# Optimization experiments

Hardware: AMD Instinct MI355X
Metric: run time of the kernel (lower is better)

The kernel has to match this reference:

```python
import jax, jax.numpy as jnp
import numpy as np

_N = 512
_L = 65536


def setup_inputs() -> dict:
    key = jax.random.key(0)
    ks = jax.random.split(key, 11)
    N, L = _N, _L
    sc = 1.0 / np.sqrt(N)  # lecun-normal style scaling
    f = lambda k, s: jax.random.normal(k, s, dtype=jnp.float32)
    return {
        # stable DPLR spectrum: negative real parts
        "Lambda_re": -(jax.random.uniform(ks[0], (N,), dtype=jnp.float32) + 0.1),
        "Lambda_im": f(ks[1], (N,)),
        "p_re": f(ks[2], (N,)), "p_im": f(ks[3], (N,)),
        "q_re": f(ks[4], (N,)), "q_im": f(ks[5], (N,)),
        "Vc_re": f(ks[6], (N, N)) * sc, "Vc_im": f(ks[7], (N, N)) * sc,
        "Ct": f(ks[8], (1, N, 2)) * sc,
        "B": f(ks[9], (N, 1)) * sc,
        "log_step": jax.random.uniform(ks[10], (1,), dtype=jnp.float32)
                    * (np.log(0.1) - np.log(0.001)) + np.log(0.001),
        "L": L,
    }


def reference(Lambda_re, Lambda_im, p_re, p_im, q_re, q_im,
              Vc_re, Vc_im, Ct, B, log_step, L):
    Lambda = Lambda_re + 1j * Lambda_im            # (N,)
    p = p_re + 1j * p_im                           # (N,)
    q = q_re + 1j * q_im                           # (N,)
    Vc = Vc_re + 1j * Vc_im                        # (N,N)
    Ct_c = Ct[..., 0] + 1j * Ct[..., 1]            # (1,N)
    Bc = (Vc @ B.astype(Vc.dtype)).ravel()         # (N,) complex, B = Vc @ B
    step = jnp.exp(log_step)[0]

    # aterm = (Ct*, q*), bterm = (B, p)
    a0 = Ct_c.conj().ravel()
    a1 = q.conj()
    b0 = Bc
    b1 = p

    # roots of unity
    Omega = jnp.exp(-2j * jnp.pi * (jnp.arange(L) / L))   # (L,)
    g = (2.0 / step) * ((1.0 - Omega) / (1.0 + Omega))    # (L,) bilinear transform
    c = 2.0 / (1.0 + Omega)                               # (L,)

    # single fused Cauchy pass: resolvent (L,N) contracted with all 4 rank-1 terms
    r = 1.0 / (g[:, None] - Lambda[None, :])               # (L,N)
    terms = jnp.stack([a0 * b0, a0 * b1, a1 * b0, a1 * b1], axis=1)  # (N,4)
    K = r @ terms                                          # (L,4): k00,k01,k10,k11
    k00, k01, k10, k11 = K[:, 0], K[:, 1], K[:, 2], K[:, 3]

    atRoots = c * (k00 - k01 * (1.0 / (1.0 + k11)) * k10)  # Woodbury correction
    out = jnp.fft.ifft(atRoots, L).reshape(L)
    return out.real
```

## Files before the change

kernel.cpp:

```cpp
#include <hip/hip_runtime.h>
#include <math.h>

constexpr int WS_TERMS = 0;
constexpr int WS_ZT    = 8192;

__global__ __launch_bounds__(256) void k_setup(
    const float* __restrict__ Lr, const float* __restrict__ Li,
    const float* __restrict__ pr, const float* __restrict__ pi,
    const float* __restrict__ qr, const float* __restrict__ qi,
    const float* __restrict__ Vr, const float* __restrict__ Vi,
    const float* __restrict__ Ct, const float* __restrict__ Bv,
    float* __restrict__ terms)
{
    __shared__ float red[8];
    int n = blockIdx.x;
    int t = threadIdx.x;
    float b0 = Bv[t], b1 = Bv[t + 256];
    float sr = fmaf(Vr[n*512 + t], b0, Vr[n*512 + t + 256] * b1);
    float si = fmaf(Vi[n*512 + t], b0, Vi[n*512 + t + 256] * b1);
    #pragma unroll
    for (int off = 32; off > 0; off >>= 1) {
        sr += __shfl_down(sr, off, 64);
        si += __shfl_down(si, off, 64);
    }
    if ((t & 63) == 0) { red[(t >> 6)*2] = sr; red[(t >> 6)*2 + 1] = si; }
    __syncthreads();
    if (t == 0) {
        float b0r = red[0] + red[2] + red[4] + red[6];
        float b0i = red[1] + red[3] + red[5] + red[7];
        float a0r = Ct[2*n], a0i = -Ct[2*n+1];
        float a1r = qr[n],   a1i = -qi[n];
        float b1r = pr[n],   b1i = pi[n];
        float* tm = terms + n * 12;
        tm[0]  = Lr[n];                tm[1]  = Li[n];
        tm[2]  = a0r*b0r - a0i*b0i;    tm[3]  = a0r*b0i + a0i*b0r;
        tm[4]  = a0r*b1r - a0i*b1i;    tm[5]  = a0r*b1i + a0i*b1r;
        tm[6]  = a1r*b0r - a1i*b0i;    tm[7]  = a1r*b0i + a1i*b0r;
        tm[8]  = a1r*b1r - a1i*b1i;    tm[9]  = a1r*b1i + a1i*b1r;
        tm[10] = 0.f;                  tm[11] = 0.f;
    }
}

__global__ __launch_bounds__(1024, 8) void k_mainA(
    const float* __restrict__ terms,
    const float* __restrict__ log_step,
    float* __restrict__ ZTf)
{
    __shared__ float buf[11520];
    int tid = threadIdx.x;
    int l1  = blockIdx.x;

    {
        float4* dst = (float4*)buf;
        const float4* src = (const float4*)terms;
        for (int i = tid; i < 1536; i += 1024) dst[i] = src[i];
    }

    int u     = tid & 127;
    int chunk = tid >> 7;

    double step = exp((double)log_step[0]);
    double t2s  = 2.0 / step;
    double th0  = -6.283185307179586 * ((double)(l1 + 256*u) / 65536.0);
    float gr[2], gi[2], cr_[2], ci_[2];
    #pragma unroll
    for (int h = 0; h < 2; ++h) {
        double th = th0 - 3.141592653589793 * (double)h;
        double sn, cn; sincos(th, &sn, &cn);
        double A = 1.0 - cn, C = 1.0 + cn, Bm = -sn, D = sn;
        double inv = 1.0 / (C*C + D*D);
        gr[h]  = (float)(t2s * (A*C + Bm*D) * inv);
        gi[h]  = (float)(t2s * (Bm*C - A*D) * inv);
        cr_[h] = (float)(2.0 * C * inv);
        ci_[h] = (float)(-2.0 * D * inv);
    }
    __syncthreads();

    float ac[2][8];
    #pragma unroll
    for (int h = 0; h < 2; ++h)
        #pragma unroll
        for (int c = 0; c < 8; ++c) ac[h][c] = 0.f;

    const float4* t4 = (const float4*)buf + chunk * 64 * 3;
    #pragma unroll 2
    for (int n = 0; n < 64; ++n) {
        float4 Aq = t4[n*3 + 0];
        float4 Bq = t4[n*3 + 1];
        float4 Cq = t4[n*3 + 2];
        #pragma unroll
        for (int h = 0; h < 2; ++h) {
            float dr = gr[h] - Aq.x;
            float di = gi[h] - Aq.y;
            float dd = fmaf(dr, dr, di * di);
            float iv = __builtin_amdgcn_rcpf(dd);
            float rr = dr * iv;
            float ri = -di * iv;
            ac[h][0] = fmaf(rr, Aq.z, ac[h][0]); ac[h][0] = fmaf(-ri, Aq.w, ac[h][0]);
            ac[h][1] = fmaf(rr, Aq.w, ac[h][1]); ac[h][1] = fmaf( ri, Aq.z, ac[h][1]);
            ac[h][2] = fmaf(rr, Bq.x, ac[h][2]); ac[h][2] = fmaf(-ri, Bq.y, ac[h][2]);
            ac[h][3] = fmaf(rr, Bq.y, ac[h][3]); ac[h][3] = fmaf( ri, Bq.x, ac[h][3]);
            ac[h][4] = fmaf(rr, Bq.z, ac[h][4]); ac[h][4] = fmaf(-ri, Bq.w, ac[h][4]);
            ac[h][5] = fmaf(rr, Bq.w, ac[h][5]); ac[h][5] = fmaf( ri, Bq.z, ac[h][5]);
            ac[h][6] = fmaf(rr, Cq.x, ac[h][6]); ac[h][6] = fmaf(-ri, Cq.y, ac[h][6]);
            ac[h][7] = fmaf(rr, Cq.y, ac[h][7]); ac[h][7] = fmaf( ri, Cq.x, ac[h][7]);
        }
    }
    __syncthreads();

    if (chunk >= 4) {
        #pragma unroll
        for (int h = 0; h < 2; ++h) {
            float* p = buf + (chunk - 4) * 2304 + (u + 128*h) * 9;
            #pragma unroll
            for (int c = 0; c < 8; ++c) p[c] = ac[h][c];
        }
    }
    __syncthreads();
    if (chunk < 4) {
        #pragma unroll
        for (int h = 0; h < 2; ++h) {
            float* p = buf + chunk * 2304 + (u + 128*h) * 9;
            #pragma unroll
            for (int c = 0; c < 8; ++c) p[c] += ac[h][c];
        }
    }
    __syncthreads();

    for (int s = tid; s < 2048; s += 1024) {
        int a = (s >> 3) * 9 + (s & 7);
        float v = buf[a] + buf[2304 + a] + buf[4608 + a] + buf[6912 + a];
        buf[9216 + a] = v;
    }
    __syncthreads();

    if (tid < 256) {
        const float* rd = buf + 9216 + tid * 9;
        float s0r = rd[0], s0i = rd[1], s1r = rd[2], s1i = rd[3];
        float s2r = rd[4], s2i = rd[5], s3r = rd[6], s3i = rd[7];
        int h = tid >> 7;
        float e1r = 1.f + s3r, e1i = s3i;
        float eiv = 1.0f / fmaf(e1r, e1r, e1i * e1i);
        float m_r = s1r * s2r - s1i * s2i;
        float m_i = s1r * s2i + s1i * s2r;
        float q_r = (m_r * e1r + m_i * e1i) * eiv;
        float q_i = (m_i * e1r - m_r * e1i) * eiv;
        float u_r = s0r - q_r;
        float u_i = s0i - q_i;
        float at_r = cr_[h] * u_r - ci_[h] * u_i;
        float at_i = cr_[h] * u_i + ci_[h] * u_r;
        ((float2*)buf)[tid] = make_float2(at_r, at_i);
    }
    __syncthreads();

    {
        int k = tid & 255;
        int s = tid >> 8;
        int m0 = (s * k) & 3;
        float curR = (m0 == 0) ? 1.f : (m0 == 2 ? -1.f : 0.f);
        float curI = (m0 == 1) ? 1.f : (m0 == 3 ? -1.f : 0.f);
        double rs, rc;
        sincos(6.283185307179586 * ((double)k / 256.0), &rs, &rc);
        float rotR = (float)rc, rotI = (float)rs;
        const float2* xrow = (const float2*)buf;
        float yr = 0.f, yi = 0.f;
        #pragma unroll 8
        for (int j = s * 64; j < s * 64 + 64; ++j) {
            float2 x = xrow[j];
            yr = fmaf(x.x, curR, yr); yr = fmaf(-x.y, curI, yr);
            yi = fmaf(x.x, curI, yi); yi = fmaf( x.y, curR, yi);
            float nR = curR * rotR - curI * rotI;
            float nI = curR * rotI + curI * rotR;
            curR = nR; curI = nI;
        }
        ((float2*)(buf + 512))[tid] = make_float2(yr, yi);
    }
    __syncthreads();
    if (tid < 256) {
        const float2* pA = (const float2*)(buf + 512);
        float2 p0 = pA[tid], p1 = pA[tid+256], p2 = pA[tid+512], p3 = pA[tid+768];
        float Yr = p0.x + p1.x + p2.x + p3.x;
        float Yi = p0.y + p1.y + p2.y + p3.y;
        int mm = (l1 * tid) & 65535;
        float tv = (float)mm * (1.0f / 65536.0f);
        float twR = __builtin_amdgcn_cosf(tv);
        float twI = __builtin_amdgcn_sinf(tv);
        ((float2*)ZTf)[tid * 256 + l1] =
            make_float2(Yr * twR - Yi * twI, Yr * twI + Yi * twR);
    }
}

__global__ __launch_bounds__(1024) void k_fftB(
    const float* __restrict__ ZTf, float* __restrict__ out)
{
    __shared__ float2 zrow[256];
    __shared__ float partB[1024];
    int t1  = blockIdx.x;
    int tid = threadIdx.x;
    if (tid < 256) zrow[tid] = ((const float2*)ZTf)[t1 * 256 + tid];
    int k   = tid & 255;
    int s   = tid >> 8;
    int m0 = (s * k) & 3;
    float curR = (m0 == 0) ? 1.f : (m0 == 2 ? -1.f : 0.f);
    float curI = (m0 == 1) ? 1.f : (m0 == 3 ? -1.f : 0.f);
    double rs, rc;
    sincos(6.283185307179586 * ((double)k / 256.0), &rs, &rc);
    float rotR = (float)rc, rotI = (float)rs;
    __syncthreads();
    float o = 0.f;
    #pragma unroll 8
    for (int j = s * 64; j < s * 64 + 64; ++j) {
        float2 z = zrow[j];
        o = fmaf(z.x, curR, o);
        o = fmaf(-z.y, curI, o);
        float nR = curR * rotR - curI * rotI;
        float nI = curR * rotI + curI * rotR;
        curR = nR; curI = nI;
    }
    partB[tid] = o;
    __syncthreads();
    if (tid < 256) {
        float sum = partB[tid] + partB[tid+256] + partB[tid+512] + partB[tid+768];
        out[t1 + 256 * tid] = sum * (1.0f / 65536.0f);
    }
}

extern "C" void kernel_launch(void* const* d_in, const int* in_sizes, int n_in,
                              void* d_out, int out_size, void* d_ws, size_t ws_size,
                              hipStream_t stream)
{
    const float* Lambda_re = (const float*)d_in[0];
    const float* Lambda_im = (const float*)d_in[1];
    const float* p_re      = (const float*)d_in[2];
    const float* p_im      = (const float*)d_in[3];
    const float* q_re      = (const float*)d_in[4];
    const float* q_im      = (const float*)d_in[5];
    const float* Vc_re     = (const float*)d_in[6];
    const float* Vc_im     = (const float*)d_in[7];
    const float* Ct        = (const float*)d_in[8];
    const float* Bv        = (const float*)d_in[9];
    const float* log_step  = (const float*)d_in[10];

    float* wsf   = (float*)d_ws;
    float* terms = wsf + WS_TERMS;
    float* ZT    = wsf + WS_ZT;
    float* out   = (float*)d_out;

    k_setup<<<512, 256, 0, stream>>>(Lambda_re, Lambda_im, p_re, p_im, q_re, q_im,
                                     Vc_re, Vc_im, Ct, Bv, terms);
    k_mainA<<<256, 1024, 0, stream>>>(terms, log_step, ZT);
    k_fftB<<<256, 1024, 0, stream>>>(ZT, out);
}
```

Measured before the change: 107.3 us.

## Fuse setup, Cauchy and FFT stages into one cooperative kernel with analytic bilinear simplification

Merges the three kernels into a single cooperative launch that uses grid-wide syncs between the setup, Cauchy/first-FFT and second-FFT phases, which removes two kernel launch gaps. It also simplifies the bilinear transform algebraically: g becomes purely imaginary (t2s·tan), so the resolvent denominator uses a precomputed Lambda_re squared, and c·u becomes (1 + iT)·u. Double-precision sincos is replaced with hardware sin/cos intrinsics. This adds grid-sync overhead and some float precision risk near the tan singularity, which is handled with a clamp.

```diff
diff --git a/kernel.cpp b/kernel.cpp
--- a/kernel.cpp
+++ b/kernel.cpp
@@ -1,86 +1,89 @@
 #include <hip/hip_runtime.h>
+#include <hip/hip_cooperative_groups.h>
 #include <math.h>
+
+namespace cg = cooperative_groups;
 
 constexpr int WS_TERMS = 0;
 constexpr int WS_ZT    = 8192;
 
-__global__ __launch_bounds__(256) void k_setup(
+__device__ __forceinline__ float sin2pi(float x) { return __builtin_amdgcn_sinf(x); }
+__device__ __forceinline__ float cos2pi(float x) { return __builtin_amdgcn_cosf(x); }
+
+__global__ __launch_bounds__(1024, 4) void k_all(
     const float* __restrict__ Lr, const float* __restrict__ Li,
     const float* __restrict__ pr, const float* __restrict__ pi,
     const float* __restrict__ qr, const float* __restrict__ qi,
     const float* __restrict__ Vr, const float* __restrict__ Vi,
     const float* __restrict__ Ct, const float* __restrict__ Bv,
-    float* __restrict__ terms)
-{
-    __shared__ float red[8];
-    int n = blockIdx.x;
-    int t = threadIdx.x;
-    float b0 = Bv[t], b1 = Bv[t + 256];
-    float sr = fmaf(Vr[n*512 + t], b0, Vr[n*512 + t + 256] * b1);
-    float si = fmaf(Vi[n*512 + t], b0, Vi[n*512 + t + 256] * b1);
-    #pragma unroll
-    for (int off = 32; off > 0; off >>= 1) {
-        sr += __shfl_down(sr, off, 64);
-        si += __shfl_down(si, off, 64);
-    }
-    if ((t & 63) == 0) { red[(t >> 6)*2] = sr; red[(t >> 6)*2 + 1] = si; }
-    __syncthreads();
-    if (t == 0) {
-        float b0r = red[0] + red[2] + red[4] + red[6];
-        float b0i = red[1] + red[3] + red[5] + red[7];
-        float a0r = Ct[2*n], a0i = -Ct[2*n+1];
-        float a1r = qr[n],   a1i = -qi[n];
-        float b1r = pr[n],   b1i = pi[n];
-        float* tm = terms + n * 12;
-        tm[0]  = Lr[n];                tm[1]  = Li[n];
-        tm[2]  = a0r*b0r - a0i*b0i;    tm[3]  = a0r*b0i + a0i*b0r;
-        tm[4]  = a0r*b1r - a0i*b1i;    tm[5]  = a0r*b1i + a0i*b1r;
-        tm[6]  = a1r*b0r - a1i*b0i;    tm[7]  = a1r*b0i + a1i*b0r;
-        tm[8]  = a1r*b1r - a1i*b1i;    tm[9]  = a1r*b1i + a1i*b1r;
-        tm[10] = 0.f;                  tm[11] = 0.f;
-    }
-}
-
-__global__ __launch_bounds__(1024, 8) void k_mainA(
-    const float* __restrict__ terms,
     const float* __restrict__ log_step,
-    float* __restrict__ ZTf)
+    float* __restrict__ termsG, float* __restrict__ ZTf,
+    float* __restrict__ out)
 {
     __shared__ float buf[11520];
+    __shared__ float red[16][2];
+    cg::grid_group grid = cg::this_grid();
     int tid = threadIdx.x;
-    int l1  = blockIdx.x;
-
+    int b   = blockIdx.x;
+
+    {
+        int half = tid >> 9;
+        int m    = tid & 511;
+        int n    = 2*b + half;
+        float bv = Bv[m];
+        float sr = Vr[n*512 + m] * bv;
+        float si = Vi[n*512 + m] * bv;
+        #pragma unroll
+        for (int off = 32; off > 0; off >>= 1) {
+            sr += __shfl_down(sr, off, 64);
+            si += __shfl_down(si, off, 64);
+        }
+        if ((tid & 63) == 0) { red[tid >> 6][0] = sr; red[tid >> 6][1] = si; }
+        __syncthreads();
+        if ((tid & 511) == 0) {
+            int wb = half * 8;
+            float b0r = 0.f, b0i = 0.f;
+            #pragma unroll
+            for (int w = 0; w < 8; ++w) { b0r += red[wb+w][0]; b0i += red[wb+w][1]; }
+            double step = exp((double)log_step[0]);
+            float t2s = (float)(2.0 / step);
+            float lr  = Lr[n];
+            float a0r = Ct[2*n], a0i = -Ct[2*n+1];
+            float a1r = qr[n],   a1i = -qi[n];
+            float b1r = pr[n],   b1i = pi[n];
+            float* tm = termsG + n * 12;
+            tm[0]  = -lr;                 tm[1]  = Li[n];
+            tm[2]  = a0r*b0r - a0i*b0i;   tm[3]  = a0r*b0i + a0i*b0r;
+            tm[4]  = a0r*b1r - a0i*b1i;   tm[5]  = a0r*b1i + a0i*b1r;
+            tm[6]  = a1r*b0r - a1i*b0i;   tm[7]  = a1r*b0i + a1i*b0r;
+            tm[8]  = a1r*b1r - a1i*b1i;   tm[9]  = a1r*b1i + a1i*b1r;
+            tm[10] = lr*lr;               tm[11] = t2s;
+        }
+    }
+    grid.sync();
+
+    int l1 = b;
     {
         float4* dst = (float4*)buf;
-        const float4* src = (const float4*)terms;
+        const float4* src = (const float4*)termsG;
         for (int i = tid; i < 1536; i += 1024) dst[i] = src[i];
     }
-
     int u     = tid & 127;
     int chunk = tid >> 7;
 
-    double step = exp((double)log_step[0]);
-    double t2s  = 2.0 / step;
-    double th0  = -6.283185307179586 * ((double)(l1 + 256*u) / 65536.0);
-    float gr[2], gi[2], cr_[2], ci_[2];
+    float tv2 = (float)(l1 + 256*u) * (1.0f / 131072.0f);
+    float sn  = sin2pi(tv2), cn = cos2pi(tv2);
+    float T0  = sn / cn;
+    float T1  = -1.0f / T0;
+    __syncthreads();
+    float t2s = buf[11];
+    float gi0 = t2s * T0, Tc0 = T0;
+    float gi1 = t2s * T1, Tc1 = T1;
+    if (!isfinite(gi1)) { gi1 = 3e30f; Tc1 = 0.f; }
+
+    float2 ac[8];
     #pragma unroll
-    for (int h = 0; h < 2; ++h) {
-        double th = th0 - 3.141592653589793 * (double)h;
-        double sn, cn; sincos(th, &sn, &cn);
-        double A = 1.0 - cn, C = 1.0 + cn, Bm = -sn, D = sn;
-        double inv = 1.0 / (C*C + D*D);
-        gr[h]  = (float)(t2s * (A*C + Bm*D) * inv);
-        gi[h]  = (float)(t2s * (Bm*C - A*D) * inv);
-        cr_[h] = (float)(2.0 * C * inv);
-        ci_[h] = (float)(-2.0 * D * inv);
-    }
-    __syncthreads();
-
-    float ac[2][8];
-    #pragma unroll
-    for (int h = 0; h < 2; ++h)
-        #pragma unroll
-        for (int c = 0; c < 8; ++c) ac[h][c] = 0.f;
+    for (int c = 0; c < 8; ++c) ac[c] = make_float2(0.f, 0.f);
 
     const float4* t4 = (const float4*)buf + chunk * 64 * 3;
     #pragma unroll 2
@@ -88,49 +91,53 @@
         float4 Aq = t4[n*3 + 0];
         float4 Bq = t4[n*3 + 1];
         float4 Cq = t4[n*3 + 2];
+        float di0 = gi0 - Aq.y;
+        float dd0 = fmaf(di0, di0, Cq.z);
+        float iv0 = __builtin_amdgcn_rcpf(dd0);
+        float rr0 = Aq.x * iv0;
+        float ri0 = -di0 * iv0;
+        ac[0].x = fmaf(rr0, Aq.z, ac[0].x); ac[0].x = fmaf(-ri0, Aq.w, ac[0].x);
+        ac[1].x = fmaf(rr0, Aq.w, ac[1].x); ac[1].x = fmaf( ri0, Aq.z, ac[1].x);
+        ac[2].x = fmaf(rr0, Bq.x, ac[2].x); ac[2].x = fmaf(-ri0, Bq.y, ac[2].x);
+        ac[3].x = fmaf(rr0, Bq.y, ac[3].x); ac[3].x = fmaf( ri0, Bq.x, ac[3].x);
+        ac[4].x = fmaf(rr0, Bq.z, ac[4].x); ac[4].x = fmaf(-ri0, Bq.w, ac[4].x);
+        ac[5].x = fmaf(rr0, Bq.w, ac[5].x); ac[5].x = fmaf( ri0, Bq.z, ac[5].x);
+        ac[6].x = fmaf(rr0, Cq.x, ac[6].x); ac[6].x = fmaf(-ri0, Cq.y, ac[6].x);
+        ac[7].x = fmaf(rr0, Cq.y, ac[7].x); ac[7].x = fmaf( ri0, Cq.x, ac[7].x);
+        float di1 = gi1 - Aq.y;
+        float dd1 = fmaf(di1, di1, Cq.z);
+        float iv1 = __builtin_amdgcn_rcpf(dd1);
+        float rr1 = Aq.x * iv1;
+        float ri1 = -di1 * iv1;
+        ac[0].y = fmaf(rr1, Aq.z, ac[0].y); ac[0].y = fmaf(-ri1, Aq.w, ac[0].y);
+        ac[1].y = fmaf(rr1, Aq.w, ac[1].y); ac[1].y = fmaf( ri1, Aq.z, ac[1].y);
+        ac[2].y = fmaf(rr1, Bq.x, ac[2].y); ac[2].y = fmaf(-ri1, Bq.y, ac[2].y);
+        ac[3].y = fmaf(rr1, Bq.y, ac[3].y); ac[3].y = fmaf( ri1, Bq.x, ac[3].y);
+        ac[4].y = fmaf(rr1, Bq.z, ac[4].y); ac[4].y = fmaf(-ri1, Bq.w, ac[4].y);
+        ac[5].y = fmaf(rr1, Bq.w, ac[5].y); ac[5].y = fmaf( ri1, Bq.z, ac[5].y);
+        ac[6].y = fmaf(rr1, Cq.x, ac[6].y); ac[6].y = fmaf(-ri1, Cq.y, ac[6].y);
+        ac[7].y = fmaf(rr1, Cq.y, ac[7].y); ac[7].y = fmaf( ri1, Cq.x, ac[7].y);
+    }
+    __syncthreads();
+
+    if (chunk >= 4) {
+        float* p0 = buf + (chunk - 4) * 2304 + u * 9;
+        float* p1 = buf + (chunk - 4) * 2304 + (u + 128) * 9;
         #pragma unroll
-        for (int h = 0; h < 2; ++h) {
-            float dr = gr[h] - Aq.x;
-            float di = gi[h] - Aq.y;
-            float dd = fmaf(dr, dr, di * di);
-            float iv = __builtin_amdgcn_rcpf(dd);
-            float rr = dr * iv;
-            float ri = -di * iv;
-            ac[h][0] = fmaf(rr, Aq.z, ac[h][0]); ac[h][0] = fmaf(-ri, Aq.w, ac[h][0]);
-            ac[h][1] = fmaf(rr, Aq.w, ac[h][1]); ac[h][1] = fmaf( ri, Aq.z, ac[h][1]);
-            ac[h][2] = fmaf(rr, Bq.x, ac[h][2]); ac[h][2] = fmaf(-ri, Bq.y, ac[h][2]);
-            ac[h][3] = fmaf(rr, Bq.y, ac[h][3]); ac[h][3] = fmaf( ri, Bq.x, ac[h][3]);
-            ac[h][4] = fmaf(rr, Bq.z, ac[h][4]); ac[h][4] = fmaf(-ri, Bq.w, ac[h][4]);
-            ac[h][5] = fmaf(rr, Bq.w, ac[h][5]); ac[h][5] = fmaf( ri, Bq.z, ac[h][5]);
-            ac[h][6] = fmaf(rr, Cq.x, ac[h][6]); ac[h][6] = fmaf(-ri, Cq.y, ac[h][6]);
-            ac[h][7] = fmaf(rr, Cq.y, ac[h][7]); ac[h][7] = fmaf( ri, Cq.x, ac[h][7]);
-        }
-    }
-    __syncthreads();
-
-    if (chunk >= 4) {
+        for (int c = 0; c < 8; ++c) { p0[c] = ac[c].x; p1[c] = ac[c].y; }
+    }
+    __syncthreads();
+    if (chunk < 4) {
+        float* p0 = buf + chunk * 2304 + u * 9;
+        float* p1 = buf + chunk * 2304 + (u + 128) * 9;
         #pragma unroll
-        for (int h = 0; h < 2; ++h) {
-            float* p = buf + (chunk - 4) * 2304 + (u + 128*h) * 9;
-            #pragma unroll
-            for (int c = 0; c < 8; ++c) p[c] = ac[h][c];
-        }
-    }
-    __syncthreads();
-    if (chunk < 4) {
-        #pragma unroll
-        for (int h = 0; h < 2; ++h) {
-            float* p = buf + chunk * 2304 + (u + 128*h) * 9;
-            #pragma unroll
-            for (int c = 0; c < 8; ++c) p[c] += ac[h][c];
-        }
+        for (int c = 0; c < 8; ++c) { p0[c] += ac[c].x; p1[c] += ac[c].y; }
     }
     __syncthreads();
 
     for (int s = tid; s < 2048; s += 1024) {
         int a = (s >> 3) * 9 + (s & 7);
-        float v = buf[a] + buf[2304 + a] + buf[4608 + a] + buf[6912 + a];
-        buf[9216 + a] = v;
+        buf[9216 + a] = buf[a] + buf[2304 + a] + buf[4608 + a] + buf[6912 + a];
     }
     __syncthreads();
 
@@ -138,7 +145,7 @@
         const float* rd = buf + 9216 + tid * 9;
         float s0r = rd[0], s0i = rd[1], s1r = rd[2], s1i = rd[3];
         float s2r = rd[4], s2i = rd[5], s3r = rd[6], s3i = rd[7];
-        int h = tid >> 7;
+        float T = (tid >> 7) ? Tc1 : Tc0;
         float e1r = 1.f + s3r, e1i = s3i;
         float eiv = 1.0f / fmaf(e1r, e1r, e1i * e1i);
         float m_r = s1r * s2r - s1i * s2i;
@@ -147,9 +154,7 @@
         float q_i = (m_i * e1r - m_r * e1i) * eiv;
         float u_r = s0r - q_r;
         float u_i = s0i - q_i;
-        float at_r = cr_[h] * u_r - ci_[h] * u_i;
-        float at_i = cr_[h] * u_i + ci_[h] * u_r;
-        ((float2*)buf)[tid] = make_float2(at_r, at_i);
+        ((float2*)buf)[tid] = make_float2(u_r - T * u_i, u_i + T * u_r);
     }
     __syncthreads();
 
@@ -159,9 +164,8 @@
         int m0 = (s * k) & 3;
         float curR = (m0 == 0) ? 1.f : (m0 == 2 ? -1.f : 0.f);
         float curI = (m0 == 1) ? 1.f : (m0 == 3 ? -1.f : 0.f);
-        double rs, rc;
-        sincos(6.283185307179586 * ((double)k / 256.0), &rs, &rc);
-        float rotR = (float)rc, rotI = (float)rs;
+        float rotR = cos2pi((float)k * (1.0f / 256.0f));
+        float rotI = sin2pi((float)k * (1.0f / 256.0f));
         const float2* xrow = (const float2*)buf;
         float yr = 0.f, yi = 0.f;
         #pragma unroll 8
@@ -183,45 +187,40 @@
         float Yi = p0.y + p1.y + p2.y + p3.y;
         int mm = (l1 * tid) & 65535;
         float tv = (float)mm * (1.0f / 65536.0f);
-        float twR = __builtin_amdgcn_cosf(tv);
-        float twI = __builtin_amdgcn_sinf(tv);
+        float twR = cos2pi(tv), twI = sin2pi(tv);
         ((float2*)ZTf)[tid * 256 + l1] =
             make_float2(Yr * twR - Yi * twI, Yr * twI + Yi * twR);
     }
-}
-
-__global__ __launch_bounds__(1024) void k_fftB(
-    const float* __restrict__ ZTf, float* __restrict__ out)
-{
-    __shared__ float2 zrow[256];
-    __shared__ float partB[1024];
-    int t1  = blockIdx.x;
-    int tid = threadIdx.x;
-    if (tid < 256) zrow[tid] = ((const float2*)ZTf)[t1 * 256 + tid];
-    int k   = tid & 255;
-    int s   = tid >> 8;
-    int m0 = (s * k) & 3;
-    float curR = (m0 == 0) ? 1.f : (m0 == 2 ? -1.f : 0.f);
-    float curI = (m0 == 1) ? 1.f : (m0 == 3 ? -1.f : 0.f);
-    double rs, rc;
-    sincos(6.283185307179586 * ((double)k / 256.0), &rs, &rc);
-    float rotR = (float)rc, rotI = (float)rs;
-    __syncthreads();
-    float o = 0.f;
-    #pragma unroll 8
-    for (int j = s * 64; j < s * 64 + 64; ++j) {
-        float2 z = zrow[j];
-        o = fmaf(z.x, curR, o);
-        o = fmaf(-z.y, curI, o);
-        float nR = curR * rotR - curI * rotI;
-        float nI = curR * rotI + curI * rotR;
-        curR = nR; curI = nI;
-    }
-    partB[tid] = o;
-    __syncthreads();
-    if (tid < 256) {
-        float sum = partB[tid] + partB[tid+256] + partB[tid+512] + partB[tid+768];
-        out[t1 + 256 * tid] = sum * (1.0f / 65536.0f);
+    grid.sync();
+
+    {
+        int t1 = b;
+        if (tid < 256) ((float2*)buf)[tid] = ((const float2*)ZTf)[t1 * 256 + tid];
+        int k = tid & 255;
+        int s = tid >> 8;
+        int m0 = (s * k) & 3;
+        float curR = (m0 == 0) ? 1.f : (m0 == 2 ? -1.f : 0.f);
+        float curI = (m0 == 1) ? 1.f : (m0 == 3 ? -1.f : 0.f);
+        float rotR = cos2pi((float)k * (1.0f / 256.0f));
+        float rotI = sin2pi((float)k * (1.0f / 256.0f));
+        __syncthreads();
+        const float2* zrow = (const float2*)buf;
+        float o = 0.f;
+        #pragma unroll 8
+        for (int j = s * 64; j < s * 64 + 64; ++j) {
+            float2 z = zrow[j];
+            o = fmaf(z.x, curR, o);
+            o = fmaf(-z.y, curI, o);
+            float nR = curR * rotR - curI * rotI;
+            float nI = curR * rotI + curI * rotR;
+            curR = nR; curI = nI;
+        }
+        buf[512 + tid] = o;
+        __syncthreads();
+        if (tid < 256) {
+            float sum = buf[512+tid] + buf[512+tid+256] + buf[512+tid+512] + buf[512+tid+768];
+            out[t1 + 256 * tid] = sum * (1.0f / 65536.0f);
+        }
     }
 }
 
@@ -244,10 +243,13 @@
     float* wsf   = (float*)d_ws;
     float* terms = wsf + WS_TERMS;
     float* ZT    = wsf + WS_ZT;
-    float* out   = (float*)d_out;
-
-    k_setup<<<512, 256, 0, stream>>>(Lambda_re, Lambda_im, p_re, p_im, q_re, q_im,
-                                     Vc_re, Vc_im, Ct, Bv, terms);
-    k_mainA<<<256, 1024, 0, stream>>>(terms, log_step, ZT);
-    k_fftB<<<256, 1024, 0, stream>>>(ZT, out);
+    float* outp  = (float*)d_out;
+
+    void* args[] = {
+        (void*)&Lambda_re, (void*)&Lambda_im, (void*)&p_re, (void*)&p_im,
+        (void*)&q_re, (void*)&q_im, (void*)&Vc_re, (void*)&Vc_im,
+        (void*)&Ct, (void*)&Bv, (void*)&log_step,
+        (void*)&terms, (void*)&ZT, (void*)&outp
+    };
+    hipLaunchCooperativeKernel((void*)k_all, dim3(256), dim3(1024), args, 0, stream);
 }
```

Result: slower. 178.3 us (+66.1%).

## Exploit bilinear-transform structure: purely imaginary g, quarter-split blocks, fp32 twiddles

Applied to the files above, without the earlier changes.

Uses the identity that (1-Omega)/(1+Omega) is purely imaginary, i*tan(theta/2). The resolvent denominator becomes |Lambda_re|^2 + (g_i - Lambda_im)^2 with precomputed terms, and the c factor becomes (1 + i*tan). This replaces the double-precision sincos setup and halves per-element arithmetic. Work is reshaped so each block handles a quarter of the 256-point inner DFT. The partial DFTs go to four workspace slices that k_fftB sums, giving 4x more, smaller blocks for both kernels. Double sincos calls are replaced with hardware sin/cos. The risk is precision near the tan singularity, which is handled by a large sentinel value, and extra workspace traffic.

```diff
diff --git a/kernel.cpp b/kernel.cpp
--- a/kernel.cpp
+++ b/kernel.cpp
@@ -3,6 +3,9 @@
 
 constexpr int WS_TERMS = 0;
 constexpr int WS_ZT    = 8192;
+
+__device__ __forceinline__ float sin2pi(float x) { return __builtin_amdgcn_sinf(x); }
+__device__ __forceinline__ float cos2pi(float x) { return __builtin_amdgcn_cosf(x); }
 
 __global__ __launch_bounds__(256) void k_setup(
     const float* __restrict__ Lr, const float* __restrict__ Li,
@@ -10,6 +13,7 @@
     const float* __restrict__ qr, const float* __restrict__ qi,
     const float* __restrict__ Vr, const float* __restrict__ Vi,
     const float* __restrict__ Ct, const float* __restrict__ Bv,
+    const float* __restrict__ log_step,
     float* __restrict__ terms)
 {
     __shared__ float red[8];
@@ -28,117 +32,101 @@
     if (t == 0) {
         float b0r = red[0] + red[2] + red[4] + red[6];
         float b0i = red[1] + red[3] + red[5] + red[7];
+        double step = exp((double)log_step[0]);
+        float t2s = (float)(2.0 / step);
+        float lr  = Lr[n];
         float a0r = Ct[2*n], a0i = -Ct[2*n+1];
         float a1r = qr[n],   a1i = -qi[n];
         float b1r = pr[n],   b1i = pi[n];
         float* tm = terms + n * 12;
-        tm[0]  = Lr[n];                tm[1]  = Li[n];
-        tm[2]  = a0r*b0r - a0i*b0i;    tm[3]  = a0r*b0i + a0i*b0r;
-        tm[4]  = a0r*b1r - a0i*b1i;    tm[5]  = a0r*b1i + a0i*b1r;
-        tm[6]  = a1r*b0r - a1i*b0i;    tm[7]  = a1r*b0i + a1i*b0r;
-        tm[8]  = a1r*b1r - a1i*b1i;    tm[9]  = a1r*b1i + a1i*b1r;
-        tm[10] = 0.f;                  tm[11] = 0.f;
-    }
-}
-
-__global__ __launch_bounds__(1024, 8) void k_mainA(
+        tm[0]  = -lr;                 tm[1]  = Li[n];
+        tm[2]  = a0r*b0r - a0i*b0i;   tm[3]  = a0r*b0i + a0i*b0r;
+        tm[4]  = a0r*b1r - a0i*b1i;   tm[5]  = a0r*b1i + a0i*b1r;
+        tm[6]  = a1r*b0r - a1i*b0i;   tm[7]  = a1r*b0i + a1i*b0r;
+        tm[8]  = a1r*b1r - a1i*b1i;   tm[9]  = a1r*b1i + a1i*b1r;
+        tm[10] = lr*lr;               tm[11] = t2s;
+    }
+}
+
+__global__ __launch_bounds__(512, 8) void k_mainA(
     const float* __restrict__ terms,
-    const float* __restrict__ log_step,
     float* __restrict__ ZTf)
 {
-    __shared__ float buf[11520];
+    __shared__ float buf[6144];
     int tid = threadIdx.x;
-    int l1  = blockIdx.x;
+    int b   = blockIdx.x;
+    int l1      = b >> 2;
+    int quarter = b & 3;
 
     {
         float4* dst = (float4*)buf;
         const float4* src = (const float4*)terms;
-        for (int i = tid; i < 1536; i += 1024) dst[i] = src[i];
-    }
-
-    int u     = tid & 127;
-    int chunk = tid >> 7;
-
-    double step = exp((double)log_step[0]);
-    double t2s  = 2.0 / step;
-    double th0  = -6.283185307179586 * ((double)(l1 + 256*u) / 65536.0);
-    float gr[2], gi[2], cr_[2], ci_[2];
+        #pragma unroll
+        for (int i = 0; i < 3; ++i) dst[tid + 512*i] = src[tid + 512*i];
+    }
+
+    int u     = tid & 63;
+    int chunk = tid >> 6;
+    int l2    = quarter*64 + u;
+    int l     = l1 + 256*l2;
+
+    float tv2 = (float)l * (1.0f / 131072.0f);
+    float sn  = sin2pi(tv2), cn = cos2pi(tv2);
+    float T   = sn / cn;
+    __syncthreads();
+    float t2s = buf[11];
+    float g_i = t2s * T;
+    if (!(fabsf(T) <= 1.0e6f)) { g_i = 3e30f; T = 0.f; }
+
+    float ac[8];
     #pragma unroll
-    for (int h = 0; h < 2; ++h) {
-        double th = th0 - 3.141592653589793 * (double)h;
-        double sn, cn; sincos(th, &sn, &cn);
-        double A = 1.0 - cn, C = 1.0 + cn, Bm = -sn, D = sn;
-        double inv = 1.0 / (C*C + D*D);
-        gr[h]  = (float)(t2s * (A*C + Bm*D) * inv);
-        gi[h]  = (float)(t2s * (Bm*C - A*D) * inv);
-        cr_[h] = (float)(2.0 * C * inv);
-        ci_[h] = (float)(-2.0 * D * inv);
-    }
-    __syncthreads();
-
-    float ac[2][8];
-    #pragma unroll
-    for (int h = 0; h < 2; ++h)
-        #pragma unroll
-        for (int c = 0; c < 8; ++c) ac[h][c] = 0.f;
+    for (int c = 0; c < 8; ++c) ac[c] = 0.f;
 
     const float4* t4 = (const float4*)buf + chunk * 64 * 3;
-    #pragma unroll 2
+    #pragma unroll 4
     for (int n = 0; n < 64; ++n) {
         float4 Aq = t4[n*3 + 0];
         float4 Bq = t4[n*3 + 1];
         float4 Cq = t4[n*3 + 2];
-        #pragma unroll
-        for (int h = 0; h < 2; ++h) {
-            float dr = gr[h] - Aq.x;
-            float di = gi[h] - Aq.y;
-            float dd = fmaf(dr, dr, di * di);
-            float iv = __builtin_amdgcn_rcpf(dd);
-            float rr = dr * iv;
-            float ri = -di * iv;
-            ac[h][0] = fmaf(rr, Aq.z, ac[h][0]); ac[h][0] = fmaf(-ri, Aq.w, ac[h][0]);
-            ac[h][1] = fmaf(rr, Aq.w, ac[h][1]); ac[h][1] = fmaf( ri, Aq.z, ac[h][1]);
-            ac[h][2] = fmaf(rr, Bq.x, ac[h][2]); ac[h][2] = fmaf(-ri, Bq.y, ac[h][2]);
-            ac[h][3] = fmaf(rr, Bq.y, ac[h][3]); ac[h][3] = fmaf( ri, Bq.x, ac[h][3]);
-            ac[h][4] = fmaf(rr, Bq.z, ac[h][4]); ac[h][4] = fmaf(-ri, Bq.w, ac[h][4]);
-            ac[h][5] = fmaf(rr, Bq.w, ac[h][5]); ac[h][5] = fmaf( ri, Bq.z, ac[h][5]);
-            ac[h][6] = fmaf(rr, Cq.x, ac[h][6]); ac[h][6] = fmaf(-ri, Cq.y, ac[h][6]);
-            ac[h][7] = fmaf(rr, Cq.y, ac[h][7]); ac[h][7] = fmaf( ri, Cq.x, ac[h][7]);
-        }
+        float di = g_i - Aq.y;
+        float dd = fmaf(di, di, Cq.z);
+        float iv = __builtin_amdgcn_rcpf(dd);
+        float rr = Aq.x * iv;
+        float ri = -di * iv;
+        ac[0] = fmaf(rr, Aq.z, ac[0]); ac[0] = fmaf(-ri, Aq.w, ac[0]);
+        ac[1] = fmaf(rr, Aq.w, ac[1]); ac[1] = fmaf( ri, Aq.z, ac[1]);
+        ac[2] = fmaf(rr, Bq.x, ac[2]); ac[2] = fmaf(-ri, Bq.y, ac[2]);
+        ac[3] = fmaf(rr, Bq.y, ac[3]); ac[3] = fmaf( ri, Bq.x, ac[3]);
+        ac[4] = fmaf(rr, Bq.z, ac[4]); ac[4] = fmaf(-ri, Bq.w, ac[4]);
+        ac[5] = fmaf(rr, Bq.w, ac[5]); ac[5] = fmaf( ri, Bq.z, ac[5]);
+        ac[6] = fmaf(rr, Cq.x, ac[6]); ac[6] = fmaf(-ri, Cq.y, ac[6]);
+        ac[7] = fmaf(rr, Cq.y, ac[7]); ac[7] = fmaf( ri, Cq.x, ac[7]);
     }
     __syncthreads();
 
     if (chunk >= 4) {
-        #pragma unroll
-        for (int h = 0; h < 2; ++h) {
-            float* p = buf + (chunk - 4) * 2304 + (u + 128*h) * 9;
-            #pragma unroll
-            for (int c = 0; c < 8; ++c) p[c] = ac[h][c];
-        }
+        float* p = buf + (chunk - 4) * 576 + u * 9;
+        #pragma unroll
+        for (int c = 0; c < 8; ++c) p[c] = ac[c];
     }
     __syncthreads();
     if (chunk < 4) {
-        #pragma unroll
-        for (int h = 0; h < 2; ++h) {
-            float* p = buf + chunk * 2304 + (u + 128*h) * 9;
-            #pragma unroll
-            for (int c = 0; c < 8; ++c) p[c] += ac[h][c];
-        }
-    }
-    __syncthreads();
-
-    for (int s = tid; s < 2048; s += 1024) {
-        int a = (s >> 3) * 9 + (s & 7);
-        float v = buf[a] + buf[2304 + a] + buf[4608 + a] + buf[6912 + a];
-        buf[9216 + a] = v;
-    }
-    __syncthreads();
-
-    if (tid < 256) {
-        const float* rd = buf + 9216 + tid * 9;
+        float* p = buf + chunk * 576 + u * 9;
+        #pragma unroll
+        for (int c = 0; c < 8; ++c) p[c] += ac[c];
+    }
+    __syncthreads();
+
+    {
+        int a = (tid >> 3) * 9 + (tid & 7);
+        buf[2304 + a] = buf[a] + buf[576 + a] + buf[1152 + a] + buf[1728 + a];
+    }
+    __syncthreads();
+
+    if (tid < 64) {
+        const float* rd = buf + 2304 + tid * 9;
         float s0r = rd[0], s0i = rd[1], s1r = rd[2], s1i = rd[3];
         float s2r = rd[4], s2i = rd[5], s3r = rd[6], s3i = rd[7];
-        int h = tid >> 7;
         float e1r = 1.f + s3r, e1i = s3i;
         float eiv = 1.0f / fmaf(e1r, e1r, e1i * e1i);
         float m_r = s1r * s2r - s1i * s2i;
@@ -147,25 +135,23 @@
         float q_i = (m_i * e1r - m_r * e1i) * eiv;
         float u_r = s0r - q_r;
         float u_i = s0i - q_i;
-        float at_r = cr_[h] * u_r - ci_[h] * u_i;
-        float at_i = cr_[h] * u_i + ci_[h] * u_r;
-        ((float2*)buf)[tid] = make_float2(at_r, at_i);
-    }
-    __syncthreads();
-
-    {
-        int k = tid & 255;
-        int s = tid >> 8;
-        int m0 = (s * k) & 3;
-        float curR = (m0 == 0) ? 1.f : (m0 == 2 ? -1.f : 0.f);
-        float curI = (m0 == 1) ? 1.f : (m0 == 3 ? -1.f : 0.f);
-        double rs, rc;
-        sincos(6.283185307179586 * ((double)k / 256.0), &rs, &rc);
-        float rotR = (float)rc, rotI = (float)rs;
+        ((float2*)buf)[tid] = make_float2(u_r - T * u_i, u_i + T * u_r);
+    }
+    __syncthreads();
+
+    {
+        int t1 = tid & 255;
+        int s  = tid >> 8;
+        int j0 = s * 32;
+        int mm0 = ((quarter*64 + j0) * t1) & 255;
+        float curR = cos2pi((float)mm0 * (1.0f/256.0f));
+        float curI = sin2pi((float)mm0 * (1.0f/256.0f));
+        float rotR = cos2pi((float)t1 * (1.0f/256.0f));
+        float rotI = sin2pi((float)t1 * (1.0f/256.0f));
         const float2* xrow = (const float2*)buf;
         float yr = 0.f, yi = 0.f;
         #pragma unroll 8
-        for (int j = s * 64; j < s * 64 + 64; ++j) {
+        for (int j = j0; j < j0 + 32; ++j) {
             float2 x = xrow[j];
             yr = fmaf(x.x, curR, yr); yr = fmaf(-x.y, curI, yr);
             yi = fmaf(x.x, curI, yi); yi = fmaf( x.y, curR, yi);
@@ -173,40 +159,49 @@
             float nI = curR * rotI + curI * rotR;
             curR = nR; curI = nI;
         }
-        ((float2*)(buf + 512))[tid] = make_float2(yr, yi);
+        ((float2*)(buf + 128))[tid] = make_float2(yr, yi);
     }
     __syncthreads();
     if (tid < 256) {
-        const float2* pA = (const float2*)(buf + 512);
-        float2 p0 = pA[tid], p1 = pA[tid+256], p2 = pA[tid+512], p3 = pA[tid+768];
-        float Yr = p0.x + p1.x + p2.x + p3.x;
-        float Yi = p0.y + p1.y + p2.y + p3.y;
+        const float2* pA = (const float2*)(buf + 128);
+        float2 p0 = pA[tid], p1 = pA[tid + 256];
+        float Yr = p0.x + p1.x;
+        float Yi = p0.y + p1.y;
         int mm = (l1 * tid) & 65535;
         float tv = (float)mm * (1.0f / 65536.0f);
-        float twR = __builtin_amdgcn_cosf(tv);
-        float twI = __builtin_amdgcn_sinf(tv);
-        ((float2*)ZTf)[tid * 256 + l1] =
+        float twR = cos2pi(tv), twI = sin2pi(tv);
+        ((float2*)(ZTf + quarter * 131072))[tid * 256 + l1] =
             make_float2(Yr * twR - Yi * twI, Yr * twI + Yi * twR);
     }
 }
 
-__global__ __launch_bounds__(1024) void k_fftB(
+__global__ __launch_bounds__(256) void k_fftB(
     const float* __restrict__ ZTf, float* __restrict__ out)
 {
-    __shared__ float2 zrow[256];
-    __shared__ float partB[1024];
-    int t1  = blockIdx.x;
+    __shared__ float buf2[768];
     int tid = threadIdx.x;
-    if (tid < 256) zrow[tid] = ((const float2*)ZTf)[t1 * 256 + tid];
-    int k   = tid & 255;
-    int s   = tid >> 8;
-    int m0 = (s * k) & 3;
+    int b   = blockIdx.x;
+    int t1 = b >> 2;
+    int qT = b & 3;
+    {
+        float2 z = make_float2(0.f, 0.f);
+        #pragma unroll
+        for (int q = 0; q < 4; ++q) {
+            float2 v = ((const float2*)(ZTf + q * 131072))[t1 * 256 + tid];
+            z.x += v.x; z.y += v.y;
+        }
+        ((float2*)buf2)[tid] = z;
+    }
+    int k2 = tid & 63;
+    int s  = tid >> 6;
+    int t2 = qT * 64 + k2;
+    int m0 = (s * t2) & 3;
     float curR = (m0 == 0) ? 1.f : (m0 == 2 ? -1.f : 0.f);
     float curI = (m0 == 1) ? 1.f : (m0 == 3 ? -1.f : 0.f);
-    double rs, rc;
-    sincos(6.283185307179586 * ((double)k / 256.0), &rs, &rc);
-    float rotR = (float)rc, rotI = (float)rs;
-    __syncthreads();
+    float rotR = cos2pi((float)t2 * (1.0f / 256.0f));
+    float rotI = sin2pi((float)t2 * (1.0f / 256.0f));
+    __syncthreads();
+    const float2* zrow = (const float2*)buf2;
     float o = 0.f;
     #pragma unroll 8
     for (int j = s * 64; j < s * 64 + 64; ++j) {
@@ -217,11 +212,11 @@
         float nI = curR * rotI + curI * rotR;
         curR = nR; curI = nI;
     }
-    partB[tid] = o;
-    __syncthreads();
-    if (tid < 256) {
-        float sum = partB[tid] + partB[tid+256] + partB[tid+512] + partB[tid+768];
-        out[t1 + 256 * tid] = sum * (1.0f / 65536.0f);
+    buf2[512 + tid] = o;
+    __syncthreads();
+    if (tid < 64) {
+        float sum = buf2[512+tid] + buf2[512+tid+64] + buf2[512+tid+128] + buf2[512+tid+192];
+        out[t1 + 256 * (qT * 64 + tid)] = sum * (1.0f / 65536.0f);
     }
 }
 
@@ -244,10 +239,10 @@
     float* wsf   = (float*)d_ws;
     float* terms = wsf + WS_TERMS;
     float* ZT    = wsf + WS_ZT;
-    float* out   = (float*)d_out;
+    float* outp  = (float*)d_out;
 
     k_setup<<<512, 256, 0, stream>>>(Lambda_re, Lambda_im, p_re, p_im, q_re, q_im,
-                                     Vc_re, Vc_im, Ct, Bv, terms);
-    k_mainA<<<256, 1024, 0, stream>>>(terms, log_step, ZT);
-    k_fftB<<<256, 1024, 0, stream>>>(ZT, out);
-}
+                                     Vc_re, Vc_im, Ct, Bv, log_step, terms);
+    k_mainA<<<1024, 512, 0, stream>>>(terms, ZT);
+    k_fftB<<<1024, 256, 0, stream>>>(ZT, outp);
+}
```

Measured after the change: 106.6 us, median of 2. Within noise of the previous version (-0.6%).
